# Kernel optimization log

Hardware: AMD Instinct MI355X
Metric: run time of the kernel (lower is better)

The kernel has to match this reference:

```python
import jax, jax.numpy as jnp
import numpy as np

SMOOTH = 1e-05

def setup_inputs() -> dict:
    key = jax.random.key(0)
    k1, k2 = jax.random.split(key)
    H = W = 2048
    C = 4
    pred = jax.random.normal(k1, (1, C, H, W), dtype=jnp.float32)
    true = jax.random.randint(k2, (H, W), 0, C, dtype=jnp.int64)
    return {"pred": pred, "true": true}


def reference(pred, true):
    # true: [H,W] int labels; pred: [1,C,H,W] logits
    C = pred.shape[1]
    p_lbl = jnp.argmax(pred, axis=1).squeeze()          # [H,W]
    t1h = jax.nn.one_hot(true, C, dtype=pred.dtype)     # [H,W,C]
    p1h = jax.nn.one_hot(p_lbl, C, dtype=pred.dtype)    # [H,W,C]

    inter = jnp.einsum('hwc,hwc->c', t1h, p1h)           # per-class intersection
    t_sum = t1h.sum(axis=(0, 1))                         # per-class true counts
    p_sum = p1h.sum(axis=(0, 1))                         # per-class pred counts

    dice = 1.0 - (2.0 * inter + SMOOTH) / (p_sum + t_sum + SMOOTH)
    # Original uses GLOBAL pred.sum()/true.sum() (over all classes) in IoU denom
    total = p1h.sum() + t1h.sum()
    iou = 1.0 - (inter + SMOOTH) / (total + SMOOTH - inter)

    # Only classes present in `true` contribute (the `if true[:,:,i].max() > 0` branch)
    present = t_sum > 0
    n = jnp.maximum(present.sum(), 1).astype(pred.dtype)
    dice_mean = jnp.where(present, dice, 0.0).sum() / n
    iou_mean = jnp.where(present, iou, 0.0).sum() / n
    return dice_mean + iou_mean
```

## Files before the change

kernel.cpp:

```cpp
#include <hip/hip_runtime.h>

static constexpr int HW   = 2048 * 2048;
static constexpr int NQ   = HW / 4;
static constexpr int NBLK = 2048;
static constexpr int NTHR = 256;
static constexpr int QPT  = NQ / (NBLK * NTHR);


__global__ __launch_bounds__(NTHR) void count_kernel(const float* __restrict__ pred,
                                                     const int* __restrict__ lbl,
                                                     unsigned int* __restrict__ partial) {
    const float4* __restrict__ p0 = (const float4*)(pred);
    const float4* __restrict__ p1 = (const float4*)(pred + (size_t)HW);
    const float4* __restrict__ p2 = (const float4*)(pred + (size_t)2 * HW);
    const float4* __restrict__ p3 = (const float4*)(pred + (size_t)3 * HW);
    const int4*   __restrict__ tl = (const int4*)(lbl);

    unsigned int pc = 0u, tc = 0u, ic = 0u;

    const int base = blockIdx.x * NTHR + threadIdx.x;
#pragma unroll
    for (int q = 0; q < QPT; ++q) {
        const int i = base + q * (NBLK * NTHR);
        float4 a = p0[i];
        float4 b = p1[i];
        float4 c = p2[i];
        float4 d = p3[i];
        int4   t = tl[i];

        float a_[4] = {a.x, a.y, a.z, a.w};
        float b_[4] = {b.x, b.y, b.z, b.w};
        float c_[4] = {c.x, c.y, c.z, c.w};
        float d_[4] = {d.x, d.y, d.z, d.w};
        int   t_[4] = {t.x, t.y, t.z, t.w};

#pragma unroll
        for (int j = 0; j < 4; ++j) {
            float best = a_[j];
            int   pi   = 0;
            if (b_[j] > best) { best = b_[j]; pi = 1; }
            if (c_[j] > best) { best = c_[j]; pi = 2; }
            if (d_[j] > best) { best = d_[j]; pi = 3; }
            int tj = t_[j];
            pc += 1u << (pi * 8);
            tc += 1u << (tj * 8);
            ic += (pi == tj) ? (1u << (pi * 8)) : 0u;
        }
    }

    unsigned int plo = pc & 0x00FF00FFu, phi = (pc >> 8) & 0x00FF00FFu;
    unsigned int tlo = tc & 0x00FF00FFu, thi = (tc >> 8) & 0x00FF00FFu;
    unsigned int ilo = ic & 0x00FF00FFu, ihi = (ic >> 8) & 0x00FF00FFu;

#pragma unroll
    for (int off = 32; off > 0; off >>= 1) {
        plo += __shfl_down(plo, off);
        phi += __shfl_down(phi, off);
        tlo += __shfl_down(tlo, off);
        thi += __shfl_down(thi, off);
        ilo += __shfl_down(ilo, off);
        ihi += __shfl_down(ihi, off);
    }

    __shared__ unsigned int red[NTHR / 64][6];
    int wave = threadIdx.x >> 6;
    int lane = threadIdx.x & 63;
    if (lane == 0) {
        red[wave][0] = plo; red[wave][1] = phi;
        red[wave][2] = tlo; red[wave][3] = thi;
        red[wave][4] = ilo; red[wave][5] = ihi;
    }
    __syncthreads();

    if (threadIdx.x == 0) {
        unsigned int s[6];
#pragma unroll
        for (int k = 0; k < 6; ++k) {
            unsigned int acc = 0;
#pragma unroll
            for (int w = 0; w < NTHR / 64; ++w) acc += red[w][k];
            s[k] = acc;
        }
        unsigned int* out = partial + (size_t)blockIdx.x * 12;
        out[0]  = s[0] & 0xFFFFu;
        out[1]  = s[1] & 0xFFFFu;
        out[2]  = s[0] >> 16;
        out[3]  = s[1] >> 16;
        out[4]  = s[2] & 0xFFFFu;
        out[5]  = s[3] & 0xFFFFu;
        out[6]  = s[2] >> 16;
        out[7]  = s[3] >> 16;
        out[8]  = s[4] & 0xFFFFu;
        out[9]  = s[5] & 0xFFFFu;
        out[10] = s[4] >> 16;
        out[11] = s[5] >> 16;
    }
}

__global__ __launch_bounds__(NTHR) void finalize_kernel(const unsigned int* __restrict__ partial,
                                                        float* __restrict__ out) {
    unsigned int s[12];
#pragma unroll
    for (int k = 0; k < 12; ++k) s[k] = 0u;

    for (int b = threadIdx.x; b < NBLK; b += NTHR) {
        const unsigned int* src = partial + (size_t)b * 12;
#pragma unroll
        for (int k = 0; k < 12; ++k) s[k] += src[k];
    }

#pragma unroll
    for (int off = 32; off > 0; off >>= 1) {
#pragma unroll
        for (int k = 0; k < 12; ++k) s[k] += __shfl_down(s[k], off);
    }

    __shared__ unsigned int red[NTHR / 64][12];
    int wave = threadIdx.x >> 6;
    int lane = threadIdx.x & 63;
    if (lane == 0) {
#pragma unroll
        for (int k = 0; k < 12; ++k) red[wave][k] = s[k];
    }
    __syncthreads();

    if (threadIdx.x == 0) {
        float p[4], t[4], in[4];
        float sp = 0.f, st = 0.f;
        unsigned int tot[12];
#pragma unroll
        for (int k = 0; k < 12; ++k) {
            unsigned int acc = 0;
#pragma unroll
            for (int w = 0; w < NTHR / 64; ++w) acc += red[w][k];
            tot[k] = acc;
        }
#pragma unroll
        for (int c = 0; c < 4; ++c) {
            p[c]  = (float)tot[c];
            t[c]  = (float)tot[4 + c];
            in[c] = (float)tot[8 + c];
            sp += p[c];
            st += t[c];
        }
        const float S = 1e-5f;
        float total = sp + st;
        float dsum = 0.f, isum = 0.f;
        int npres = 0;
#pragma unroll
        for (int c = 0; c < 4; ++c) {
            if (tot[4 + c] > 0u) {
                ++npres;
                dsum += 1.0f - (2.0f * in[c] + S) / (p[c] + t[c] + S);
                isum += 1.0f - (in[c] + S) / (total + S - in[c]);
            }
        }
        float n = (float)(npres > 0 ? npres : 1);
        out[0] = dsum / n + isum / n;
    }
}

extern "C" void kernel_launch(void* const* d_in, const int* in_sizes, int n_in,
                              void* d_out, int out_size, void* d_ws, size_t ws_size,
                              hipStream_t stream) {
    const float* pred = (const float*)d_in[0];
    const int*   lbl  = (const int*)d_in[1];
    float*       out  = (float*)d_out;
    unsigned int* partial = (unsigned int*)d_ws;

    count_kernel<<<NBLK, NTHR, 0, stream>>>(pred, lbl, partial);
    finalize_kernel<<<1, NTHR, 0, stream>>>(partial, out);
}
```

Measured before the change: 24.91 us.

## Fuse finalize into count kernel via last-block atomic ticket

Replaces the separate single-block finalize kernel with a last-block-done pattern: each block writes its partial counts as uint4 rows, fences, and takes an atomic ticket, and the final block performs the global reduction and the metric computation. This is meant to remove the second kernel launch and its dependency gap. In exchange it adds a memset of the counter before each launch and a serial tail on one block. Partial writes are also vectorized to uint4.

```diff
diff --git a/kernel.cpp b/kernel.cpp
--- a/kernel.cpp
+++ b/kernel.cpp
@@ -6,15 +6,18 @@
 static constexpr int NTHR = 256;
 static constexpr int QPT  = NQ / (NBLK * NTHR);
 
+static constexpr size_t PART_OFF = 64;
 
 __global__ __launch_bounds__(NTHR) void count_kernel(const float* __restrict__ pred,
                                                      const int* __restrict__ lbl,
-                                                     unsigned int* __restrict__ partial) {
+                                                     unsigned int* __restrict__ ws,
+                                                     float* __restrict__ out) {
     const float4* __restrict__ p0 = (const float4*)(pred);
     const float4* __restrict__ p1 = (const float4*)(pred + (size_t)HW);
     const float4* __restrict__ p2 = (const float4*)(pred + (size_t)2 * HW);
     const float4* __restrict__ p3 = (const float4*)(pred + (size_t)3 * HW);
     const int4*   __restrict__ tl = (const int4*)(lbl);
+    uint4* __restrict__ partial = (uint4*)((char*)ws + PART_OFF);
 
     unsigned int pc = 0u, tc = 0u, ic = 0u;
 
@@ -63,6 +66,7 @@
     }
 
     __shared__ unsigned int red[NTHR / 64][6];
+    __shared__ int last_flag;
     int wave = threadIdx.x >> 6;
     int lane = threadIdx.x & 63;
     if (lane == 0) {
@@ -81,32 +85,30 @@
             for (int w = 0; w < NTHR / 64; ++w) acc += red[w][k];
             s[k] = acc;
         }
-        unsigned int* out = partial + (size_t)blockIdx.x * 12;
-        out[0]  = s[0] & 0xFFFFu;
-        out[1]  = s[1] & 0xFFFFu;
-        out[2]  = s[0] >> 16;
-        out[3]  = s[1] >> 16;
-        out[4]  = s[2] & 0xFFFFu;
-        out[5]  = s[3] & 0xFFFFu;
-        out[6]  = s[2] >> 16;
-        out[7]  = s[3] >> 16;
-        out[8]  = s[4] & 0xFFFFu;
-        out[9]  = s[5] & 0xFFFFu;
-        out[10] = s[4] >> 16;
-        out[11] = s[5] >> 16;
+        uint4 r0 = make_uint4(s[0] & 0xFFFFu, s[1] & 0xFFFFu, s[0] >> 16, s[1] >> 16);
+        uint4 r1 = make_uint4(s[2] & 0xFFFFu, s[3] & 0xFFFFu, s[2] >> 16, s[3] >> 16);
+        uint4 r2 = make_uint4(s[4] & 0xFFFFu, s[5] & 0xFFFFu, s[4] >> 16, s[5] >> 16);
+        uint4* row = partial + (size_t)blockIdx.x * 3;
+        row[0] = r0; row[1] = r1; row[2] = r2;
+        __threadfence();
+        unsigned int ticket = atomicAdd(ws, 1u);
+        last_flag = (ticket == (unsigned int)(NBLK - 1)) ? 1 : 0;
     }
-}
+    __syncthreads();
+    if (!last_flag) return;
 
-__global__ __launch_bounds__(NTHR) void finalize_kernel(const unsigned int* __restrict__ partial,
-                                                        float* __restrict__ out) {
+    __threadfence();
+
     unsigned int s[12];
 #pragma unroll
     for (int k = 0; k < 12; ++k) s[k] = 0u;
 
     for (int b = threadIdx.x; b < NBLK; b += NTHR) {
-        const unsigned int* src = partial + (size_t)b * 12;
-#pragma unroll
-        for (int k = 0; k < 12; ++k) s[k] += src[k];
+        const uint4* row = partial + (size_t)b * 3;
+        uint4 r0 = row[0], r1 = row[1], r2 = row[2];
+        s[0] += r0.x; s[1] += r0.y; s[2]  += r0.z; s[3]  += r0.w;
+        s[4] += r1.x; s[5] += r1.y; s[6]  += r1.z; s[7]  += r1.w;
+        s[8] += r2.x; s[9] += r2.y; s[10] += r2.z; s[11] += r2.w;
     }
 
 #pragma unroll
@@ -115,26 +117,24 @@
         for (int k = 0; k < 12; ++k) s[k] += __shfl_down(s[k], off);
     }
 
-    __shared__ unsigned int red[NTHR / 64][12];
-    int wave = threadIdx.x >> 6;
-    int lane = threadIdx.x & 63;
+    __shared__ unsigned int red2[NTHR / 64][12];
     if (lane == 0) {
 #pragma unroll
-        for (int k = 0; k < 12; ++k) red[wave][k] = s[k];
+        for (int k = 0; k < 12; ++k) red2[wave][k] = s[k];
     }
     __syncthreads();
 
     if (threadIdx.x == 0) {
-        float p[4], t[4], in[4];
-        float sp = 0.f, st = 0.f;
         unsigned int tot[12];
 #pragma unroll
         for (int k = 0; k < 12; ++k) {
             unsigned int acc = 0;
 #pragma unroll
-            for (int w = 0; w < NTHR / 64; ++w) acc += red[w][k];
+            for (int w = 0; w < NTHR / 64; ++w) acc += red2[w][k];
             tot[k] = acc;
         }
+        float p[4], t[4], in[4];
+        float sp = 0.f, st = 0.f;
 #pragma unroll
         for (int c = 0; c < 4; ++c) {
             p[c]  = (float)tot[c];
@@ -166,8 +166,8 @@
     const float* pred = (const float*)d_in[0];
     const int*   lbl  = (const int*)d_in[1];
     float*       out  = (float*)d_out;
-    unsigned int* partial = (unsigned int*)d_ws;
+    unsigned int* ws  = (unsigned int*)d_ws;
 
-    count_kernel<<<NBLK, NTHR, 0, stream>>>(pred, lbl, partial);
-    finalize_kernel<<<1, NTHR, 0, stream>>>(partial, out);
+    hipMemsetAsync(ws, 0, sizeof(unsigned int), stream);
+    count_kernel<<<NBLK, NTHR, 0, stream>>>(pred, lbl, ws, out);
 }
```

After: 88.63 us. 3.56x slower.
